# Performance work log

Hardware: AMD Instinct MI355X
Metric: run time of the kernel (lower is better)

The kernel has to match this reference:

```python
import jax, jax.numpy as jnp
import numpy as np

N, E, F_IN, HID, HEADS, OUT_DIM, G = 50000, 600000, 92, 32, 8, 1, 512
EPS = 1e-5


def setup_inputs() -> dict:
    key = jax.random.key(0)
    ks = jax.random.split(key, 30)
    s = 0.1
    d1 = HID * HEADS  # 256
    inp = {
        "x": jax.random.normal(ks[0], (N, F_IN), dtype=jnp.float32),
        "edge_index": jax.random.randint(ks[1], (2, E), 0, N),
        "edge_attr": jax.random.uniform(ks[2], (E, 1), dtype=jnp.float32),
        "batch": jnp.sort(jax.random.randint(ks[3], (N,), 0, G)),
        # conv1 (heads=8, concat)
        "W1": jax.random.normal(ks[4], (F_IN, d1)) * s,
        "We1": jax.random.normal(ks[5], (1, d1)) * s,
        "as1": jax.random.normal(ks[6], (HEADS, HID)) * s,
        "ad1": jax.random.normal(ks[7], (HEADS, HID)) * s,
        "ae1": jax.random.normal(ks[8], (HEADS, HID)) * s,
        "b1": jax.random.normal(ks[9], (d1,)) * s,
        # bn1 (eval mode, running stats)
        "g1": jnp.ones((d1,)), "be1": jnp.zeros((d1,)),
        "m1": jax.random.normal(ks[10], (d1,)) * s, "v1": jnp.ones((d1,)),
        # conv2 (heads=1)
        "W2": jax.random.normal(ks[11], (d1, HID)) * s,
        "We2": jax.random.normal(ks[12], (1, HID)) * s,
        "as2": jax.random.normal(ks[13], (1, HID)) * s,
        "ad2": jax.random.normal(ks[14], (1, HID)) * s,
        "ae2": jax.random.normal(ks[15], (1, HID)) * s,
        "b2": jax.random.normal(ks[16], (HID,)) * s,
        # bn2
        "g2": jnp.ones((HID,)), "be2": jnp.zeros((HID,)),
        "m2": jax.random.normal(ks[17], (HID,)) * s, "v2": jnp.ones((HID,)),
        # final fc
        "fcW": jax.random.normal(ks[18], (HID, OUT_DIM)) * s,
        "fcb": jnp.zeros((OUT_DIM,)),
    }
    return inp


def _gat_conv(x, edge_index, edge_attr, W, We, a_s, a_d, a_e, b, heads, ch):
    """PyG GATConv with edge_dim, add_self_loops=True (fill_value='mean'), concat."""
    n = x.shape[0]
    src, dst = edge_index[0], edge_index[1]
    # self loops: loop edge_attr = mean of incoming edge_attr per node
    cnt = jax.ops.segment_sum(jnp.ones((edge_attr.shape[0],), edge_attr.dtype), dst, n)
    loop_attr = jax.ops.segment_sum(edge_attr, dst, n) / jnp.clip(cnt, 1.0)[:, None]
    ar = jnp.arange(n)
    src = jnp.concatenate([src, ar])
    dst = jnp.concatenate([dst, ar])
    ea = jnp.concatenate([edge_attr, loop_attr], axis=0)
    h = (x @ W).reshape(n, heads, ch)                 # [N,H,C]
    al_s = jnp.sum(h * a_s, axis=-1)                  # [N,H]
    al_d = jnp.sum(h * a_d, axis=-1)                  # [N,H]
    he = (ea @ We).reshape(-1, heads, ch)             # [E',H,C]
    al_e = jnp.sum(he * a_e, axis=-1)                 # [E',H]
    alpha = jax.nn.leaky_relu(al_s[src] + al_d[dst] + al_e, 0.2)
    # scatter softmax over destination segments
    mx = jax.ops.segment_max(alpha, dst, n)
    w = jnp.exp(alpha - mx[dst])
    den = jax.ops.segment_sum(w, dst, n)
    w = w / den[dst]                                  # [E',H]
    out = jax.ops.segment_sum(h[src] * w[:, :, None], dst, n)  # [N,H,C]
    return out.reshape(n, heads * ch) + b


def _bn_eval(x, g, b, m, v):
    return (x - m) * (g / jnp.sqrt(v + EPS)) + b


def reference(x, edge_index, edge_attr, batch,
              W1, We1, as1, ad1, ae1, b1, g1, be1, m1, v1,
              W2, We2, as2, ad2, ae2, b2, g2, be2, m2, v2,
              fcW, fcb):
    h = _gat_conv(x, edge_index, edge_attr, W1, We1, as1, ad1, ae1, b1, HEADS, HID)
    h = jax.nn.relu(_bn_eval(h, g1, be1, m1, v1))
    # dropout is identity in eval mode
    h = _gat_conv(h, edge_index, edge_attr, W2, We2, as2, ad2, ae2, b2, 1, HID)
    h = jax.nn.relu(_bn_eval(h, g2, be2, m2, v2))
    # global mean pool over graphs
    sums = jax.ops.segment_sum(h, batch, G)
    cnt = jax.ops.segment_sum(jnp.ones((h.shape[0],), h.dtype), batch, G)
    pooled = sums / jnp.clip(cnt, 1.0)[:, None]
    return pooled @ fcW + fcb
```

## Files before the change

kernel.cpp:

```cpp
#include <hip/hip_runtime.h>
#include <hip/hip_bf16.h>

#define N_NODES 50000
#define N_EDGES 600000
#define F_IN    92
#define KPAD    96
#define HID     32
#define HEADS   8
#define D1      256
#define G_GRAPHS 512
#define EPSV    1e-5f
#define NCHUNK  49

using short8  = __attribute__((ext_vector_type(8))) short;
using f32x4   = __attribute__((ext_vector_type(4))) float;

__device__ __forceinline__ float bf2f(unsigned short u) {
    return __uint_as_float(((unsigned)u) << 16);
}
__device__ __forceinline__ unsigned short f2bf(float f) {
    unsigned u = __float_as_uint(f);
    return (unsigned short)((u + 0x7FFFu + ((u >> 16) & 1u)) >> 16);
}


__global__ void k_deg(const int* __restrict__ ei, int* __restrict__ deg) {
    int e = blockIdx.x * 256 + threadIdx.x;
    if (e < N_EDGES) atomicAdd(&deg[ei[N_EDGES + e]], 1);
}

__global__ void k_partial(const int* __restrict__ deg, int* __restrict__ partials) {
    int b = blockIdx.x;
    int s = 0;
    for (int j = 0; j < 4; ++j) {
        int i = b * 1024 + j * 256 + threadIdx.x;
        if (i < N_NODES) s += deg[i];
    }
    for (int off = 32; off; off >>= 1) s += __shfl_down(s, off, 64);
    __shared__ int sm[4];
    if ((threadIdx.x & 63) == 0) sm[threadIdx.x >> 6] = s;
    __syncthreads();
    if (threadIdx.x == 0) partials[b] = sm[0] + sm[1] + sm[2] + sm[3];
}

__global__ void k_scanp(const int* __restrict__ partials, int* __restrict__ poff) {
    if (threadIdx.x == 0 && blockIdx.x == 0) {
        int acc = 0;
        for (int b = 0; b < NCHUNK; ++b) { poff[b] = acc; acc += partials[b]; }
    }
}

__global__ void k_scanc(const int* __restrict__ deg, const int* __restrict__ poff,
                        int* __restrict__ row_off, int* __restrict__ cursor) {
    int b = blockIdx.x;
    int t = threadIdx.x;
    int base_i = b * 1024 + t * 4;
    int v[4]; int s = 0;
    #pragma unroll
    for (int j = 0; j < 4; ++j) {
        int i = base_i + j;
        v[j] = (i < N_NODES) ? deg[i] : 0;
        s += v[j];
    }
    __shared__ int sm[256];
    sm[t] = s;
    __syncthreads();
    int val = s;
    for (int off = 1; off < 256; off <<= 1) {
        int add = (t >= off) ? sm[t - off] : 0;
        __syncthreads();
        val += add;
        sm[t] = val;
        __syncthreads();
    }
    int base = poff[b] + (val - s);
    #pragma unroll
    for (int j = 0; j < 4; ++j) {
        int i = base_i + j;
        if (i < N_NODES) { row_off[i] = base; cursor[i] = base; }
        base += v[j];
    }
}

__global__ void k_fill(const int* __restrict__ ei, const float* __restrict__ ea,
                       int* __restrict__ cursor, int* __restrict__ adj_src,
                       float* __restrict__ adj_ea) {
    int e = blockIdx.x * 256 + threadIdx.x;
    if (e < N_EDGES) {
        int d = ei[N_EDGES + e];
        int pos = atomicAdd(&cursor[d], 1);
        adj_src[pos] = ei[e];
        adj_ea[pos] = ea[e];
    }
}

__global__ void k_setup(const float* __restrict__ W1, const float* __restrict__ W2,
                        const float* __restrict__ We1, const float* __restrict__ ae1,
                        const float* __restrict__ We2, const float* __restrict__ ae2,
                        const float* __restrict__ as1, const float* __restrict__ ad1,
                        const float* __restrict__ b1, const float* __restrict__ g1,
                        const float* __restrict__ be1, const float* __restrict__ m1,
                        const float* __restrict__ v1,
                        const float* __restrict__ b2, const float* __restrict__ g2,
                        const float* __restrict__ be2, const float* __restrict__ m2,
                        const float* __restrict__ v2,
                        unsigned short* __restrict__ W1p, unsigned short* __restrict__ W2p,
                        float* __restrict__ va, float* __restrict__ wedot,
                        float* __restrict__ bnA1, float* __restrict__ bnB1,
                        float* __restrict__ bnA2, float* __restrict__ bnB2) {
    int b = blockIdx.x, t = threadIdx.x;
    if (b < 96) {
        int gid = b * 256 + t;
        int k = gid >> 8, col = gid & 255;
        unsigned short v = 0;
        if (k < F_IN) v = f2bf(W1[k * D1 + col]);
        W1p[(((k >> 3) * D1) + col) * 8 + (k & 7)] = v;
    } else if (b < 128) {
        int gid = (b - 96) * 256 + t;
        int k = gid >> 5, col = gid & 31;
        W2p[(((k >> 3) * 32) + col) * 8 + (k & 7)] = f2bf(W2[gid]);
    } else if (b < 134) {
        int gid = (b - 128) * 256 + t;
        if (gid < 2 * HEADS * F_IN) {
            int which = gid / (HEADS * F_IN), rem = gid % (HEADS * F_IN);
            int h = rem / F_IN, k = rem % F_IN;
            const float* av = which ? ad1 : as1;
            float s = 0.f;
            #pragma unroll 8
            for (int c = 0; c < HID; ++c) s += W1[k * D1 + h * HID + c] * av[h * HID + c];
            va[gid] = s;
        }
    } else if (b == 134) {
        if (t < HEADS) {
            float a = 0.f;
            for (int c = 0; c < HID; ++c) a += We1[t * HID + c] * ae1[t * HID + c];
            wedot[t] = a;
        } else if (t == HEADS) {
            float a = 0.f;
            for (int c = 0; c < HID; ++c) a += We2[c] * ae2[c];
            wedot[HEADS] = a;
        }
    } else {
        if (t < D1) {
            float sc = g1[t] * __frsqrt_rn(v1[t] + EPSV);
            bnA1[t] = sc;
            bnB1[t] = (b1[t] - m1[t]) * sc + be1[t];
        }
        if (t < HID) {
            float sc = g2[t] * __frsqrt_rn(v2[t] + EPSV);
            bnA2[t] = sc;
            bnB2[t] = (b2[t] - m2[t]) * sc + be2[t];
        }
    }
}

__global__ __launch_bounds__(256) void k_conv1(const float* __restrict__ x,
                                               const unsigned short* __restrict__ W1p,
                                               const float* __restrict__ va,
                                               unsigned short* __restrict__ h1,
                                               float* __restrict__ al_s,
                                               float* __restrict__ al_d) {
    __shared__ float xs[16 * F_IN];
    __shared__ unsigned short xbs[16 * KPAD];
    int n0 = blockIdx.x * 16;
    int t = threadIdx.x;
    for (int i = t; i < 16 * F_IN; i += 256)
        xs[i] = x[(size_t)n0 * F_IN + i];
    __syncthreads();
    for (int i = t; i < 16 * KPAD; i += 256) {
        int r = i / KPAD, k = i - r * KPAD;
        xbs[i] = (k < F_IN) ? f2bf(xs[r * F_IN + k]) : (unsigned short)0;
    }
    {
        int r = t >> 4, j = t & 15;
        const float* vp = va + j * F_IN;
        const float* xr = xs + r * F_IN;
        float s = 0.f;
        for (int k = 0; k < F_IN; ++k) s += xr[k] * vp[k];
        if (j < 8) al_s[(n0 + r) * HEADS + j] = s;
        else       al_d[(n0 + r) * HEADS + (j - 8)] = s;
    }
    __syncthreads();
    int wid = t >> 6, l = t & 63;
    int g = l >> 4, c16 = l & 15;
    const short8* xb = (const short8*)(xbs + c16 * KPAD + g * 8);
    short8 af0 = xb[0], af1 = xb[4], af2 = xb[8];
    const short8* wp = (const short8*)W1p;
    #pragma unroll
    for (int ct = 0; ct < 4; ++ct) {
        int col = (wid * 4 + ct) * 16 + c16;
        f32x4 acc = {0.f, 0.f, 0.f, 0.f};
        acc = __builtin_amdgcn_mfma_f32_16x16x32_bf16(af0, wp[(0 * 4 + g) * D1 + col], acc, 0, 0, 0);
        acc = __builtin_amdgcn_mfma_f32_16x16x32_bf16(af1, wp[(1 * 4 + g) * D1 + col], acc, 0, 0, 0);
        acc = __builtin_amdgcn_mfma_f32_16x16x32_bf16(af2, wp[(2 * 4 + g) * D1 + col], acc, 0, 0, 0);
        #pragma unroll
        for (int r = 0; r < 4; ++r)
            h1[(size_t)(n0 + g * 4 + r) * D1 + col] = f2bf(acc[r]);
    }
}

__global__ __launch_bounds__(256) void k_aggr1(
        const int* __restrict__ row_off, const int* __restrict__ deg,
        const int* __restrict__ adj_src, const float* __restrict__ adj_ea,
        const unsigned short* __restrict__ h1,
        const float* __restrict__ al_s, const float* __restrict__ al_d,
        const float* __restrict__ wedot,
        const float* __restrict__ bnA1, const float* __restrict__ bnB1,
        unsigned short* __restrict__ h1p) {
    int wid = threadIdx.x >> 6, l = threadIdx.x & 63;
    int n = blockIdx.x * 4 + wid;
    if (n >= N_NODES) return;
    int h = l >> 3;
    float wd = wedot[h];
    float dn = al_d[n * HEADS + h];
    int r0 = row_off[n], cnt = deg[n];
    float a0 = 0.f, a1 = 0.f, a2 = 0.f, a3 = 0.f, den = 0.f, ea_sum = 0.f;
    for (int base = 0; base < cnt; base += 64) {
        int m = cnt - base; if (m > 64) m = 64;
        int sl = 0; float el = 0.f;
        if (l < m) {
            sl = adj_src[r0 + base + l];
            el = adj_ea[r0 + base + l];
        }
        for (int i = 0; i < m; ++i) {
            int s = __shfl(sl, i, 64);
            float eav = __shfl(el, i, 64);
            float a = al_s[s * HEADS + h] + dn + eav * wd;
            a = a > 0.f ? a : 0.2f * a;
            float w = __expf(a);
            den += w;
            ea_sum += eav;
            ushort4 p = *(const ushort4*)(h1 + (size_t)s * D1 + l * 4);
            a0 += w * bf2f(p.x); a1 += w * bf2f(p.y);
            a2 += w * bf2f(p.z); a3 += w * bf2f(p.w);
        }
    }
    {
        float la = ea_sum / (float)(cnt > 0 ? cnt : 1);
        float a = al_s[n * HEADS + h] + dn + la * wd;
        a = a > 0.f ? a : 0.2f * a;
        float w = __expf(a);
        den += w;
        ushort4 p = *(const ushort4*)(h1 + (size_t)n * D1 + l * 4);
        a0 += w * bf2f(p.x); a1 += w * bf2f(p.y);
        a2 += w * bf2f(p.z); a3 += w * bf2f(p.w);
    }
    float inv = 1.f / den;
    int c = l * 4;
    float4 A = *(const float4*)(bnA1 + c);
    float4 B = *(const float4*)(bnB1 + c);
    ushort4 o;
    o.x = f2bf(fmaxf(a0 * inv * A.x + B.x, 0.f));
    o.y = f2bf(fmaxf(a1 * inv * A.y + B.y, 0.f));
    o.z = f2bf(fmaxf(a2 * inv * A.z + B.z, 0.f));
    o.w = f2bf(fmaxf(a3 * inv * A.w + B.w, 0.f));
    *(ushort4*)(h1p + (size_t)n * D1 + c) = o;
}


__global__ __launch_bounds__(256) void k_gemm2(const unsigned short* __restrict__ h1p,
                                               const unsigned short* __restrict__ W2p,
                                               const float* __restrict__ as2,
                                               const float* __restrict__ ad2,
                                               unsigned short* __restrict__ h2b,
                                               float* __restrict__ al_s2,
                                               float* __restrict__ al_d2) {
    int wid = threadIdx.x >> 6, l = threadIdx.x & 63;
    int wave = blockIdx.x * 4 + wid;
    if (wave >= N_NODES / 16) return;
    int n0 = wave * 16;
    int g = l >> 4;
    int c16 = l & 15;
    f32x4 acc0 = {0.f, 0.f, 0.f, 0.f};
    f32x4 acc1 = {0.f, 0.f, 0.f, 0.f};
    const short8* ap = (const short8*)(h1p + (size_t)(n0 + c16) * D1 + g * 8);
    const short8* wp = (const short8*)W2p;
    #pragma unroll
    for (int ks = 0; ks < 8; ++ks) {
        short8 afrag = ap[ks * 4];
        short8 b0 = wp[(ks * 4 + g) * 32 + c16];
        short8 b1 = wp[(ks * 4 + g) * 32 + 16 + c16];
        acc0 = __builtin_amdgcn_mfma_f32_16x16x32_bf16(afrag, b0, acc0, 0, 0, 0);
        acc1 = __builtin_amdgcn_mfma_f32_16x16x32_bf16(afrag, b1, acc1, 0, 0, 0);
    }
    float s0 = as2[c16], s1 = as2[16 + c16];
    float d0 = ad2[c16], d1 = ad2[16 + c16];
    float ps[4], pd[4];
    #pragma unroll
    for (int r = 0; r < 4; ++r) {
        int node = n0 + g * 4 + r;
        h2b[(size_t)node * HID + c16]      = f2bf(acc0[r]);
        h2b[(size_t)node * HID + 16 + c16] = f2bf(acc1[r]);
        ps[r] = acc0[r] * s0 + acc1[r] * s1;
        pd[r] = acc0[r] * d0 + acc1[r] * d1;
    }
    #pragma unroll
    for (int off = 1; off < 16; off <<= 1) {
        #pragma unroll
        for (int r = 0; r < 4; ++r) {
            ps[r] += __shfl_xor(ps[r], off, 64);
            pd[r] += __shfl_xor(pd[r], off, 64);
        }
    }
    if (c16 == 0) {
        #pragma unroll
        for (int r = 0; r < 4; ++r) {
            int node = n0 + g * 4 + r;
            al_s2[node] = ps[r];
            al_d2[node] = pd[r];
        }
    }
}

__global__ __launch_bounds__(256) void k_aggr2(
        const int* __restrict__ row_off, const int* __restrict__ deg,
        const int* __restrict__ adj_src, const float* __restrict__ adj_ea,
        const unsigned short* __restrict__ h2b,
        const float* __restrict__ al_s2, const float* __restrict__ al_d2,
        const float* __restrict__ wedot,
        const float* __restrict__ bnA2, const float* __restrict__ bnB2,
        float* __restrict__ h2p) {
    int wid = threadIdx.x >> 6, l = threadIdx.x & 63;
    int n = blockIdx.x * 4 + wid;
    if (n >= N_NODES) return;
    int q = l >> 4, c2 = l & 15;
    float wd = wedot[HEADS];
    float dn = al_d2[n];
    int r0 = row_off[n], cnt = deg[n];
    float acc0 = 0.f, acc1 = 0.f, den = 0.f, ea_sum = 0.f;
    for (int base = 0; base < cnt; base += 64) {
        int m = cnt - base; if (m > 64) m = 64;
        int sl = 0; float el = 0.f;
        if (l < m) {
            sl = adj_src[r0 + base + l];
            el = adj_ea[r0 + base + l];
        }
        for (int i = 0; i < m; i += 4) {
            int j = i + q;
            int jj = j < m ? j : 0;
            int s = __shfl(sl, jj, 64);
            float eav = __shfl(el, jj, 64);
            if (j < m) {
                float a = al_s2[s] + dn + eav * wd;
                a = a > 0.f ? a : 0.2f * a;
                float w = __expf(a);
                den += w;
                ea_sum += eav;
                ushort2 p = *(const ushort2*)(h2b + (size_t)s * HID + c2 * 2);
                acc0 += w * bf2f(p.x);
                acc1 += w * bf2f(p.y);
            }
        }
    }
    acc0 += __shfl_xor(acc0, 16, 64); acc0 += __shfl_xor(acc0, 32, 64);
    acc1 += __shfl_xor(acc1, 16, 64); acc1 += __shfl_xor(acc1, 32, 64);
    den  += __shfl_xor(den, 16, 64);  den  += __shfl_xor(den, 32, 64);
    ea_sum += __shfl_xor(ea_sum, 16, 64); ea_sum += __shfl_xor(ea_sum, 32, 64);
    {
        float la = ea_sum / (float)(cnt > 0 ? cnt : 1);
        float a = al_s2[n] + dn + la * wd;
        a = a > 0.f ? a : 0.2f * a;
        float w = __expf(a);
        den += w;
        ushort2 p = *(const ushort2*)(h2b + (size_t)n * HID + c2 * 2);
        acc0 += w * bf2f(p.x);
        acc1 += w * bf2f(p.y);
    }
    int c = c2 * 2;
    float inv = 1.f / den;
    float y0 = fmaxf(acc0 * inv * bnA2[c] + bnB2[c], 0.f);
    float y1 = fmaxf(acc1 * inv * bnA2[c + 1] + bnB2[c + 1], 0.f);
    if (q == 0) {
        float2 st = {y0, y1};
        *(float2*)(h2p + (size_t)n * HID + c) = st;
    }
}

__global__ __launch_bounds__(64) void k_poolfc(const float* __restrict__ h2p,
                                               const int* __restrict__ batch,
                                               const float* __restrict__ fcW,
                                               const float* __restrict__ fcb,
                                               float* __restrict__ out) {
    int g = blockIdx.x;
    int l = threadIdx.x;
    auto lb = [&](int key) {
        int lo = 0, hi = N_NODES;
        while (lo < hi) {
            int mid = (lo + hi) >> 1;
            if (batch[mid] < key) lo = mid + 1; else hi = mid;
        }
        return lo;
    };
    int s0 = lb(g), s1 = lb(g + 1);
    int c = l & 31, half = l >> 5;
    float acc = 0.f;
    for (int r = s0 + half; r < s1; r += 2)
        acc += h2p[(size_t)r * HID + c];
    acc += __shfl_xor(acc, 32, 64);
    int cn = s1 - s0;
    float mean = acc / (float)(cn > 0 ? cn : 1);
    float p = mean * fcW[c];
    #pragma unroll
    for (int off = 1; off < 32; off <<= 1) p += __shfl_xor(p, off, 64);
    if (l == 0) out[g] = p + fcb[0];
}


extern "C" void kernel_launch(void* const* d_in, const int* in_sizes, int n_in,
                              void* d_out, int out_size, void* d_ws, size_t ws_size,
                              hipStream_t stream) {
    const float* x    = (const float*)d_in[0];
    const int*   ei   = (const int*)  d_in[1];
    const float* ea   = (const float*)d_in[2];
    const int*   batch= (const int*)  d_in[3];
    const float* W1   = (const float*)d_in[4];
    const float* We1  = (const float*)d_in[5];
    const float* as1  = (const float*)d_in[6];
    const float* ad1  = (const float*)d_in[7];
    const float* ae1  = (const float*)d_in[8];
    const float* b1   = (const float*)d_in[9];
    const float* g1   = (const float*)d_in[10];
    const float* be1  = (const float*)d_in[11];
    const float* m1   = (const float*)d_in[12];
    const float* v1   = (const float*)d_in[13];
    const float* W2   = (const float*)d_in[14];
    const float* We2  = (const float*)d_in[15];
    const float* as2  = (const float*)d_in[16];
    const float* ad2  = (const float*)d_in[17];
    const float* ae2  = (const float*)d_in[18];
    const float* b2   = (const float*)d_in[19];
    const float* g2   = (const float*)d_in[20];
    const float* be2  = (const float*)d_in[21];
    const float* m2   = (const float*)d_in[22];
    const float* v2   = (const float*)d_in[23];
    const float* fcW  = (const float*)d_in[24];
    const float* fcb  = (const float*)d_in[25];
    float* out = (float*)d_out;

    char* ws = (char*)d_ws;
    size_t off = 0;
    auto alloc = [&](size_t bytes) -> void* {
        void* p = ws + off;
        off += (bytes + 255) & ~(size_t)255;
        return p;
    };
    int*   deg     = (int*)  alloc((size_t)N_NODES * 4);
    int*   row_off = (int*)  alloc((size_t)N_NODES * 4);
    int*   cursor  = (int*)  alloc((size_t)N_NODES * 4);
    int*   adj_src = (int*)  alloc((size_t)N_EDGES * 4);
    float* adj_ea  = (float*)alloc((size_t)N_EDGES * 4);
    float* al_s1   = (float*)alloc((size_t)N_NODES * HEADS * 4);
    float* al_d1   = (float*)alloc((size_t)N_NODES * HEADS * 4);
    float* al_s2   = (float*)alloc((size_t)N_NODES * 4);
    float* al_d2   = (float*)alloc((size_t)N_NODES * 4);
    float* wedot   = (float*)alloc(16 * 4);
    float* va      = (float*)alloc((size_t)2 * HEADS * F_IN * 4);
    int*   partials= (int*)  alloc(64 * 4);
    int*   poff    = (int*)  alloc(64 * 4);
    float* bnA1    = (float*)alloc((size_t)D1 * 4);
    float* bnB1    = (float*)alloc((size_t)D1 * 4);
    float* bnA2    = (float*)alloc((size_t)HID * 4);
    float* bnB2    = (float*)alloc((size_t)HID * 4);
    unsigned short* W1p = (unsigned short*)alloc((size_t)KPAD * D1 * 2);
    unsigned short* W2p = (unsigned short*)alloc((size_t)D1 * HID * 2);
    unsigned short* h1  = (unsigned short*)alloc((size_t)N_NODES * D1 * 2);
    unsigned short* h1p = (unsigned short*)alloc((size_t)N_NODES * D1 * 2);
    unsigned short* h2b = (unsigned short*)alloc((size_t)N_NODES * HID * 2);
    float* h2p     = (float*)alloc((size_t)N_NODES * HID * 4);
    (void)ws_size; (void)in_sizes; (void)n_in; (void)out_size;

    hipMemsetAsync(deg, 0, (size_t)N_NODES * 4, stream);

    k_deg<<<(N_EDGES + 255) / 256, 256, 0, stream>>>(ei, deg);
    k_partial<<<NCHUNK, 256, 0, stream>>>(deg, partials);
    k_scanp<<<1, 64, 0, stream>>>(partials, poff);
    k_scanc<<<NCHUNK, 256, 0, stream>>>(deg, poff, row_off, cursor);
    k_fill<<<(N_EDGES + 255) / 256, 256, 0, stream>>>(ei, ea, cursor, adj_src, adj_ea);
    k_setup<<<136, 256, 0, stream>>>(W1, W2, We1, ae1, We2, ae2, as1, ad1,
                                     b1, g1, be1, m1, v1, b2, g2, be2, m2, v2,
                                     W1p, W2p, va, wedot, bnA1, bnB1, bnA2, bnB2);

    k_conv1<<<N_NODES / 16, 256, 0, stream>>>(x, W1p, va, h1, al_s1, al_d1);
    k_aggr1<<<(N_NODES + 3) / 4, 256, 0, stream>>>(row_off, deg, adj_src, adj_ea,
                                                   h1, al_s1, al_d1, wedot,
                                                   bnA1, bnB1, h1p);

    k_gemm2<<<(N_NODES / 16 + 3) / 4, 256, 0, stream>>>(h1p, W2p, as2, ad2, h2b, al_s2, al_d2);
    k_aggr2<<<(N_NODES + 3) / 4, 256, 0, stream>>>(row_off, deg, adj_src, adj_ea,
                                                   h2b, al_s2, al_d2, wedot, bnA2, bnB2, h2p);
    k_poolfc<<<G_GRAPHS, 64, 0, stream>>>(h2p, batch, fcW, fcb, out);
}
```

Measured before the change: 234.5 us.

## Merge degree count with setup, fold scan into scanc, pack adjacency as int2

The degree-count atomics and the weight/BN setup now run in one launch. The single-thread partial-scan kernel is removed, and each scanc block sums the preceding chunk partials with a wavefront reduction. Source index and edge attribute are packed into one int2 adjacency array, so the fill and aggregation kernels do one 8-byte access per edge instead of two 4-byte ones. The aim is fewer kernel launches and fewer memory transactions in the edge-gather phase, at the cost of a slightly heavier scanc prologue.

```diff
diff --git a/kernel.cpp b/kernel.cpp
--- a/kernel.cpp
+++ b/kernel.cpp
@@ -11,6 +11,7 @@
 #define G_GRAPHS 512
 #define EPSV    1e-5f
 #define NCHUNK  49
+#define DEGBLK  2344
 
 using short8  = __attribute__((ext_vector_type(8))) short;
 using f32x4   = __attribute__((ext_vector_type(4))) float;
@@ -24,91 +25,29 @@
 }
 
 
-__global__ void k_deg(const int* __restrict__ ei, int* __restrict__ deg) {
-    int e = blockIdx.x * 256 + threadIdx.x;
-    if (e < N_EDGES) atomicAdd(&deg[ei[N_EDGES + e]], 1);
-}
-
-__global__ void k_partial(const int* __restrict__ deg, int* __restrict__ partials) {
-    int b = blockIdx.x;
-    int s = 0;
-    for (int j = 0; j < 4; ++j) {
-        int i = b * 1024 + j * 256 + threadIdx.x;
-        if (i < N_NODES) s += deg[i];
-    }
-    for (int off = 32; off; off >>= 1) s += __shfl_down(s, off, 64);
-    __shared__ int sm[4];
-    if ((threadIdx.x & 63) == 0) sm[threadIdx.x >> 6] = s;
-    __syncthreads();
-    if (threadIdx.x == 0) partials[b] = sm[0] + sm[1] + sm[2] + sm[3];
-}
-
-__global__ void k_scanp(const int* __restrict__ partials, int* __restrict__ poff) {
-    if (threadIdx.x == 0 && blockIdx.x == 0) {
-        int acc = 0;
-        for (int b = 0; b < NCHUNK; ++b) { poff[b] = acc; acc += partials[b]; }
-    }
-}
-
-__global__ void k_scanc(const int* __restrict__ deg, const int* __restrict__ poff,
-                        int* __restrict__ row_off, int* __restrict__ cursor) {
-    int b = blockIdx.x;
-    int t = threadIdx.x;
-    int base_i = b * 1024 + t * 4;
-    int v[4]; int s = 0;
-    #pragma unroll
-    for (int j = 0; j < 4; ++j) {
-        int i = base_i + j;
-        v[j] = (i < N_NODES) ? deg[i] : 0;
-        s += v[j];
-    }
-    __shared__ int sm[256];
-    sm[t] = s;
-    __syncthreads();
-    int val = s;
-    for (int off = 1; off < 256; off <<= 1) {
-        int add = (t >= off) ? sm[t - off] : 0;
-        __syncthreads();
-        val += add;
-        sm[t] = val;
-        __syncthreads();
-    }
-    int base = poff[b] + (val - s);
-    #pragma unroll
-    for (int j = 0; j < 4; ++j) {
-        int i = base_i + j;
-        if (i < N_NODES) { row_off[i] = base; cursor[i] = base; }
-        base += v[j];
-    }
-}
-
-__global__ void k_fill(const int* __restrict__ ei, const float* __restrict__ ea,
-                       int* __restrict__ cursor, int* __restrict__ adj_src,
-                       float* __restrict__ adj_ea) {
-    int e = blockIdx.x * 256 + threadIdx.x;
-    if (e < N_EDGES) {
-        int d = ei[N_EDGES + e];
-        int pos = atomicAdd(&cursor[d], 1);
-        adj_src[pos] = ei[e];
-        adj_ea[pos] = ea[e];
-    }
-}
-
-__global__ void k_setup(const float* __restrict__ W1, const float* __restrict__ W2,
-                        const float* __restrict__ We1, const float* __restrict__ ae1,
-                        const float* __restrict__ We2, const float* __restrict__ ae2,
-                        const float* __restrict__ as1, const float* __restrict__ ad1,
-                        const float* __restrict__ b1, const float* __restrict__ g1,
-                        const float* __restrict__ be1, const float* __restrict__ m1,
-                        const float* __restrict__ v1,
-                        const float* __restrict__ b2, const float* __restrict__ g2,
-                        const float* __restrict__ be2, const float* __restrict__ m2,
-                        const float* __restrict__ v2,
-                        unsigned short* __restrict__ W1p, unsigned short* __restrict__ W2p,
-                        float* __restrict__ va, float* __restrict__ wedot,
-                        float* __restrict__ bnA1, float* __restrict__ bnB1,
-                        float* __restrict__ bnA2, float* __restrict__ bnB2) {
-    int b = blockIdx.x, t = threadIdx.x;
+__global__ __launch_bounds__(256) void k_deg_setup(
+        const int* __restrict__ ei, int* __restrict__ deg,
+        const float* __restrict__ W1, const float* __restrict__ W2,
+        const float* __restrict__ We1, const float* __restrict__ ae1,
+        const float* __restrict__ We2, const float* __restrict__ ae2,
+        const float* __restrict__ as1, const float* __restrict__ ad1,
+        const float* __restrict__ b1, const float* __restrict__ g1,
+        const float* __restrict__ be1, const float* __restrict__ m1,
+        const float* __restrict__ v1,
+        const float* __restrict__ b2, const float* __restrict__ g2,
+        const float* __restrict__ be2, const float* __restrict__ m2,
+        const float* __restrict__ v2,
+        unsigned short* __restrict__ W1p, unsigned short* __restrict__ W2p,
+        float* __restrict__ va, float* __restrict__ wedot,
+        float* __restrict__ bnA1, float* __restrict__ bnB1,
+        float* __restrict__ bnA2, float* __restrict__ bnB2) {
+    int blk = blockIdx.x, t = threadIdx.x;
+    if (blk < DEGBLK) {
+        int e = blk * 256 + t;
+        if (e < N_EDGES) atomicAdd(&deg[ei[N_EDGES + e]], 1);
+        return;
+    }
+    int b = blk - DEGBLK;
     if (b < 96) {
         int gid = b * 256 + t;
         int k = gid >> 8, col = gid & 255;
@@ -154,6 +93,69 @@
     }
 }
 
+__global__ void k_partial(const int* __restrict__ deg, int* __restrict__ partials) {
+    int b = blockIdx.x;
+    int s = 0;
+    for (int j = 0; j < 4; ++j) {
+        int i = b * 1024 + j * 256 + threadIdx.x;
+        if (i < N_NODES) s += deg[i];
+    }
+    for (int off = 32; off; off >>= 1) s += __shfl_down(s, off, 64);
+    __shared__ int sm[4];
+    if ((threadIdx.x & 63) == 0) sm[threadIdx.x >> 6] = s;
+    __syncthreads();
+    if (threadIdx.x == 0) partials[b] = sm[0] + sm[1] + sm[2] + sm[3];
+}
+
+__global__ void k_scanc(const int* __restrict__ deg, const int* __restrict__ partials,
+                        int* __restrict__ row_off, int* __restrict__ cursor) {
+    int b = blockIdx.x;
+    int t = threadIdx.x;
+    __shared__ int smp;
+    if (t < 64) {
+        int pv = (t < b) ? partials[t] : 0;
+        #pragma unroll
+        for (int off = 32; off; off >>= 1) pv += __shfl_down(pv, off, 64);
+        if (t == 0) smp = pv;
+    }
+    int base_i = b * 1024 + t * 4;
+    int v[4]; int s = 0;
+    #pragma unroll
+    for (int j = 0; j < 4; ++j) {
+        int i = base_i + j;
+        v[j] = (i < N_NODES) ? deg[i] : 0;
+        s += v[j];
+    }
+    __shared__ int sm[256];
+    sm[t] = s;
+    __syncthreads();
+    int val = s;
+    for (int off = 1; off < 256; off <<= 1) {
+        int add = (t >= off) ? sm[t - off] : 0;
+        __syncthreads();
+        val += add;
+        sm[t] = val;
+        __syncthreads();
+    }
+    int base = smp + (val - s);
+    #pragma unroll
+    for (int j = 0; j < 4; ++j) {
+        int i = base_i + j;
+        if (i < N_NODES) { row_off[i] = base; cursor[i] = base; }
+        base += v[j];
+    }
+}
+
+__global__ void k_fill(const int* __restrict__ ei, const float* __restrict__ ea,
+                       int* __restrict__ cursor, int2* __restrict__ adj) {
+    int e = blockIdx.x * 256 + threadIdx.x;
+    if (e < N_EDGES) {
+        int d = ei[N_EDGES + e];
+        int pos = atomicAdd(&cursor[d], 1);
+        adj[pos] = make_int2(ei[e], __float_as_int(ea[e]));
+    }
+}
+
 __global__ __launch_bounds__(256) void k_conv1(const float* __restrict__ x,
                                                const unsigned short* __restrict__ W1p,
                                                const float* __restrict__ va,
@@ -201,7 +203,7 @@
 
 __global__ __launch_bounds__(256) void k_aggr1(
         const int* __restrict__ row_off, const int* __restrict__ deg,
-        const int* __restrict__ adj_src, const float* __restrict__ adj_ea,
+        const int2* __restrict__ adj,
         const unsigned short* __restrict__ h1,
         const float* __restrict__ al_s, const float* __restrict__ al_d,
         const float* __restrict__ wedot,
@@ -219,8 +221,9 @@
         int m = cnt - base; if (m > 64) m = 64;
         int sl = 0; float el = 0.f;
         if (l < m) {
-            sl = adj_src[r0 + base + l];
-            el = adj_ea[r0 + base + l];
+            int2 se = adj[r0 + base + l];
+            sl = se.x;
+            el = __int_as_float(se.y);
         }
         for (int i = 0; i < m; ++i) {
             int s = __shfl(sl, i, 64);
@@ -314,7 +317,7 @@
 
 __global__ __launch_bounds__(256) void k_aggr2(
         const int* __restrict__ row_off, const int* __restrict__ deg,
-        const int* __restrict__ adj_src, const float* __restrict__ adj_ea,
+        const int2* __restrict__ adj,
         const unsigned short* __restrict__ h2b,
         const float* __restrict__ al_s2, const float* __restrict__ al_d2,
         const float* __restrict__ wedot,
@@ -332,8 +335,9 @@
         int m = cnt - base; if (m > 64) m = 64;
         int sl = 0; float el = 0.f;
         if (l < m) {
-            sl = adj_src[r0 + base + l];
-            el = adj_ea[r0 + base + l];
+            int2 se = adj[r0 + base + l];
+            sl = se.x;
+            el = __int_as_float(se.y);
         }
         for (int i = 0; i < m; i += 4) {
             int j = i + q;
@@ -447,8 +451,7 @@
     int*   deg     = (int*)  alloc((size_t)N_NODES * 4);
     int*   row_off = (int*)  alloc((size_t)N_NODES * 4);
     int*   cursor  = (int*)  alloc((size_t)N_NODES * 4);
-    int*   adj_src = (int*)  alloc((size_t)N_EDGES * 4);
-    float* adj_ea  = (float*)alloc((size_t)N_EDGES * 4);
+    int2*  adj     = (int2*) alloc((size_t)N_EDGES * 8);
     float* al_s1   = (float*)alloc((size_t)N_NODES * HEADS * 4);
     float* al_d1   = (float*)alloc((size_t)N_NODES * HEADS * 4);
     float* al_s2   = (float*)alloc((size_t)N_NODES * 4);
@@ -456,7 +459,6 @@
     float* wedot   = (float*)alloc(16 * 4);
     float* va      = (float*)alloc((size_t)2 * HEADS * F_IN * 4);
     int*   partials= (int*)  alloc(64 * 4);
-    int*   poff    = (int*)  alloc(64 * 4);
     float* bnA1    = (float*)alloc((size_t)D1 * 4);
     float* bnB1    = (float*)alloc((size_t)D1 * 4);
     float* bnA2    = (float*)alloc((size_t)HID * 4);
@@ -471,22 +473,22 @@
 
     hipMemsetAsync(deg, 0, (size_t)N_NODES * 4, stream);
 
-    k_deg<<<(N_EDGES + 255) / 256, 256, 0, stream>>>(ei, deg);
+    k_deg_setup<<<DEGBLK + 136, 256, 0, stream>>>(ei, deg, W1, W2, We1, ae1, We2, ae2,
+                                                  as1, ad1, b1, g1, be1, m1, v1,
+                                                  b2, g2, be2, m2, v2,
+                                                  W1p, W2p, va, wedot,
+                                                  bnA1, bnB1, bnA2, bnB2);
     k_partial<<<NCHUNK, 256, 0, stream>>>(deg, partials);
-    k_scanp<<<1, 64, 0, stream>>>(partials, poff);
-    k_scanc<<<NCHUNK, 256, 0, stream>>>(deg, poff, row_off, cursor);
-    k_fill<<<(N_EDGES + 255) / 256, 256, 0, stream>>>(ei, ea, cursor, adj_src, adj_ea);
-    k_setup<<<136, 256, 0, stream>>>(W1, W2, We1, ae1, We2, ae2, as1, ad1,
-                                     b1, g1, be1, m1, v1, b2, g2, be2, m2, v2,
-                                     W1p, W2p, va, wedot, bnA1, bnB1, bnA2, bnB2);
+    k_scanc<<<NCHUNK, 256, 0, stream>>>(deg, partials, row_off, cursor);
+    k_fill<<<(N_EDGES + 255) / 256, 256, 0, stream>>>(ei, ea, cursor, adj);
 
     k_conv1<<<N_NODES / 16, 256, 0, stream>>>(x, W1p, va, h1, al_s1, al_d1);
-    k_aggr1<<<(N_NODES + 3) / 4, 256, 0, stream>>>(row_off, deg, adj_src, adj_ea,
+    k_aggr1<<<(N_NODES + 3) / 4, 256, 0, stream>>>(row_off, deg, adj,
                                                    h1, al_s1, al_d1, wedot,
                                                    bnA1, bnB1, h1p);
 
     k_gemm2<<<(N_NODES / 16 + 3) / 4, 256, 0, stream>>>(h1p, W2p, as2, ad2, h2b, al_s2, al_d2);
-    k_aggr2<<<(N_NODES + 3) / 4, 256, 0, stream>>>(row_off, deg, adj_src, adj_ea,
+    k_aggr2<<<(N_NODES + 3) / 4, 256, 0, stream>>>(row_off, deg, adj,
                                                    h2b, al_s2, al_d2, wedot, bnA2, bnB2, h2p);
     k_poolfc<<<G_GRAPHS, 64, 0, stream>>>(h2p, batch, fcW, fcb, out);
 }
```

Result: faster. 225.9 us (-3.7%).
